# Kernel tuning notes

Hardware: AMD Instinct MI355X
Metric: run time of the kernel (lower is better)

Reference implementation:

```python
import jax, jax.numpy as jnp
import numpy as np

EPS_BN = 1e-5
EPS_COS = 1e-8

N, F_IN, HID, OUT, S, NNZ = 50000, 1024, 256, 280, 5000, 800000


def setup_inputs() -> dict:
    key = jax.random.key(0)
    ks = jax.random.split(key, 20)
    inp = {}
    inp["x"] = jax.random.normal(ks[0], (N, F_IN), jnp.float32)
    inp["y"] = jax.random.normal(ks[1], (S, OUT), jnp.float32)
    inp["adj_rows"] = jax.random.randint(ks[2], (NNZ,), 0, N, jnp.int32)
    inp["adj_cols"] = jax.random.randint(ks[3], (NNZ,), 0, N, jnp.int32)
    inp["adj_vals"] = jax.random.uniform(ks[4], (NNZ,), jnp.float32)
    inp["agg_rows"] = jax.random.randint(ks[5], (N,), 0, S, jnp.int32)
    inp["agg_vals"] = jax.random.uniform(ks[6], (N,), jnp.float32)
    inp["perm"] = jax.random.permutation(ks[7], N).astype(jnp.int32)
    # parameters (kaiming-ish scale)
    def lin(k, fi, fo):
        k1, k2 = jax.random.split(k)
        w = jax.random.normal(k1, (fi, fo), jnp.float32) / np.sqrt(fi)
        b = jax.random.normal(k2, (fo,), jnp.float32) * 0.01
        return w, b
    inp["mlp_W"], inp["mlp_b"] = lin(ks[8], F_IN, HID)
    inp["bn_gamma"] = jnp.ones((HID,), jnp.float32)
    inp["bn_beta"] = jnp.zeros((HID,), jnp.float32)
    inp["hg_W1"], inp["hg_b1"] = lin(ks[9], HID, HID)
    inp["hg_W2"], inp["hg_b2"] = lin(ks[10], HID, HID)
    inp["hg_prelu"] = jnp.float32(0.25)
    inp["pred_W"], inp["pred_b"] = lin(ks[11], HID, OUT)
    inp["dgi_W"], inp["dgi_b"] = lin(ks[12], HID, OUT)
    inp["dgi_prelu"] = jnp.float32(0.25)
    return inp


def _spmm(rows, cols, vals, M, n_out):
    # sparse(H) @ M : gather source rows, scale by edge value, scatter-add to dest
    return jax.ops.segment_sum(vals[:, None] * M[cols], rows, num_segments=n_out)


def _prelu(t, a):
    return jnp.where(t >= 0, t, a * t)


def _leaky(t, s):
    return jnp.where(t >= 0, t, s * t)


def reference(x, y, adj_rows, adj_cols, adj_vals, agg_rows, agg_vals, perm,
              mlp_W, mlp_b, bn_gamma, bn_beta, hg_W1, hg_b1, hg_W2, hg_b2,
              hg_prelu, pred_W, pred_b, dgi_W, dgi_b, dgi_prelu):
    n = x.shape[0]
    s = y.shape[0]
    # mlp: Linear -> LeakyReLU(0.1) -> BatchNorm1d (batch stats, training mode)
    h0 = _leaky(x @ mlp_W + mlp_b, 0.1)
    mu = jnp.mean(h0, axis=0)
    var = jnp.mean((h0 - mu) ** 2, axis=0)  # biased, as torch BN training
    h0 = bn_gamma * (h0 - mu) * jax.lax.rsqrt(var + EPS_BN) + bn_beta
    # HGNN, num_layers=2 (dropout = identity in eval)
    t = _spmm(adj_rows, adj_cols, adj_vals, h0 @ hg_W1 + hg_b1, n)
    t = _prelu(t, hg_prelu)
    t = _spmm(adj_rows, adj_cols, adj_vals, t @ hg_W2 + hg_b2, n)
    h = _leaky(t, 0.01)
    x_prime = _leaky(h @ pred_W + pred_b, 0.01)
    # Xenium: loss = MSE(agg_mtx @ x_prime, y); agg_mtx has one nnz per cell
    agg = jax.ops.segment_sum(agg_vals[:, None] * x_prime, agg_rows, num_segments=s)
    loss = jnp.mean((agg - y) ** 2)
    # DGI (1-layer HGNN with PReLU)
    h1 = _prelu(_spmm(adj_rows, adj_cols, adj_vals, h0 @ dgi_W + dgi_b, n), dgi_prelu)
    c = jnp.mean(h1, axis=0)  # (OUT,)
    h2 = _prelu(_spmm(adj_rows, adj_cols, adj_vals, h0[perm] @ dgi_W + dgi_b, n), dgi_prelu)
    c_norm = jnp.linalg.norm(c)
    def cos(hm):
        return (hm @ c) / jnp.maximum(jnp.linalg.norm(hm, axis=1) * c_norm, EPS_COS)
    loss = loss + jnp.mean(1.0 - cos(h1)) + jnp.mean(jnp.maximum(cos(h2), 0.0))
    return (loss, x_prime)
```

## Files before the change

### kernel.cpp

```cpp
#include <hip/hip_runtime.h>
#include <hip/hip_bf16.h>

#define DEVI __device__ __forceinline__

typedef __attribute__((ext_vector_type(8))) short short8;
typedef __attribute__((ext_vector_type(4))) float float4v;

DEVI float bf2f(__hip_bfloat16 v) { return __bfloat162float(v); }
DEVI float ldbs(const ushort* p, size_t i) { return bf2f(((const __hip_bfloat16*)p)[i]); }
DEVI ushort f2bs(float v) {
    __hip_bfloat16 h = __float2bfloat16(v);
    return *(ushort*)&h;
}
DEVI float bfs2f(short s) {
    ushort u = (ushort)s;
    return bf2f(*(__hip_bfloat16*)&u);
}

DEVI float ldin(const void* p, size_t i, int isf32) {
    return isf32 ? ((const float*)p)[i] : bf2f(((const __hip_bfloat16*)p)[i]);
}
DEVI void stio(void* p, size_t i, float v, int isf32) {
    if (isf32) ((float*)p)[i] = v;
    else ((ushort*)p)[i] = f2bs(v);
}

template <int ACT>
DEVI float act_fn(float v, float alpha) {
    if (ACT == 1) return v >= 0.f ? v : 0.1f * v;
    if (ACT == 2) return v >= 0.f ? v : 0.01f * v;
    if (ACT == 3) return v >= 0.f ? v : alpha * v;
    return v;
}

DEVI float waveRed(float v) {
#pragma unroll
    for (int o = 32; o > 0; o >>= 1) v += __shfl_down(v, o);
    return v;
}

DEVI float blockRed(float v) {
    __shared__ float sm[16];
    int lane = threadIdx.x & 63, w = threadIdx.x >> 6;
    v = waveRed(v);
    if (lane == 0) sm[w] = v;
    __syncthreads();
    if (w == 0) {
        int nw = (blockDim.x + 63) >> 6;
        v = (lane < nw) ? sm[lane] : 0.f;
        v = waveRed(v);
    }
    return v;
}

__global__ void probe_k(const void* __restrict__ x, int* __restrict__ flag) {
    __shared__ int sfails;
    int t = threadIdx.x;
    if (t == 0) sfails = 0;
    __syncthreads();
    const __hip_bfloat16* xb = (const __hip_bfloat16*)x;
    int my = 0;
    for (int i = t; i < 4096; i += 256) {
        float v = bf2f(xb[i]);
        float a = fabsf(v);
        if (!(a <= 64.f) || (v != 0.f && a < 1e-6f)) my++;
    }
    atomicAdd(&sfails, my);
    __syncthreads();
    if (t == 0) flag[0] = (sfails > 409) ? 1 : 0;
}

struct Cvt5 {
    const void* src[5];
    ushort* dst[5];
    int K[5];
    int N[5];
};
__global__ void cvt_all_k(Cvt5 d, const int* __restrict__ flagp) {
    int f32 = flagp[0];
    int seg = blockIdx.y;
    int idx = blockIdx.x * blockDim.x + threadIdx.x;
    int K = d.K[seg], Nc = d.N[seg];
    int total = K * Nc;
    if (idx < total) {
        int k = idx / Nc, n = idx % Nc;
        d.dst[seg][(size_t)n * K + k] = f2bs(ldin(d.src[seg], idx, f32));
    }
}

#define TP 40
template <int AMODE, int ACT, int OMODE>
__global__ __launch_bounds__(256) void mgemm_k(
    const void* __restrict__ A, const ushort* __restrict__ Bt,
    const void* __restrict__ bias, void* __restrict__ outp, ushort* __restrict__ outp2,
    const int* __restrict__ flagp, int M, int K, int Nc) {
    __shared__ short As[128 * TP];
    __shared__ short Bs[128 * TP];
    const int f32 = flagp[0];
    const int tid = threadIdx.x;
    const int lane = tid & 63;
    const int l15 = lane & 15;
    const int quad = lane >> 4;
    const int wid = tid >> 6;
    const int mW = (wid >> 1) * 64;
    const int nW = (wid & 1) * 64;
    const int mBase = blockIdx.x * 128;
    const int nBase = blockIdx.y * 128;

    float4v acc[4][4];
#pragma unroll
    for (int i = 0; i < 4; i++)
#pragma unroll
        for (int j = 0; j < 4; j++) acc[i][j] = (float4v){0.f, 0.f, 0.f, 0.f};

    for (int k0 = 0; k0 < K; k0 += 32) {
#pragma unroll
        for (int i = 0; i < 2; i++) {
            int chunk = i * 256 + tid;
            int row = chunk >> 2;
            int c = chunk & 3;
            short8 va = {0, 0, 0, 0, 0, 0, 0, 0};
            int gr = mBase + row;
            if (gr < M) {
                size_t ge = (size_t)gr * K + k0 + c * 8;
                if (AMODE == 1 || !f32) {
                    va = *(const short8*)((const ushort*)A + ge);
                } else {
                    const float* af = (const float*)A + ge;
#pragma unroll
                    for (int j = 0; j < 8; j++) va[j] = (short)f2bs(af[j]);
                }
            }
            *(short8*)&As[row * TP + c * 8] = va;

            short8 vb = {0, 0, 0, 0, 0, 0, 0, 0};
            int gn = nBase + row;
            if (gn < Nc) vb = *(const short8*)(Bt + (size_t)gn * K + k0 + c * 8);
            *(short8*)&Bs[row * TP + c * 8] = vb;
        }
        __syncthreads();

        short8 af[4], bf[4];
#pragma unroll
        for (int i = 0; i < 4; i++)
            af[i] = *(const short8*)&As[(mW + i * 16 + l15) * TP + quad * 8];
#pragma unroll
        for (int j = 0; j < 4; j++)
            bf[j] = *(const short8*)&Bs[(nW + j * 16 + l15) * TP + quad * 8];
#pragma unroll
        for (int i = 0; i < 4; i++)
#pragma unroll
            for (int j = 0; j < 4; j++)
                acc[i][j] =
                    __builtin_amdgcn_mfma_f32_16x16x32_bf16(af[i], bf[j], acc[i][j], 0, 0, 0);
        __syncthreads();
    }

#pragma unroll
    for (int i = 0; i < 4; i++) {
#pragma unroll
        for (int j = 0; j < 4; j++) {
            int gcn = nBase + nW + j * 16 + l15;
            if (gcn >= Nc) continue;
            float bv = ldin(bias, gcn, f32);
#pragma unroll
            for (int r = 0; r < 4; r++) {
                int grm = mBase + mW + i * 16 + quad * 4 + r;
                if (grm >= M) continue;
                float v = act_fn<ACT>(acc[i][j][r] + bv, 0.f);
                size_t oi = (size_t)grm * Nc + gcn;
                if (OMODE == 1) {
                    stio(outp, 1 + oi, v, f32);
                    outp2[oi] = f2bs(v);
                } else {
                    ((ushort*)outp)[oi] = f2bs(v);
                }
            }
        }
    }
}

__global__ void count_k(const int* __restrict__ rows, int* __restrict__ counts, int nnz) {
    int i = blockIdx.x * blockDim.x + threadIdx.x;
    if (i < nnz) atomicAdd(&counts[rows[i]], 1);
}

__global__ __launch_bounds__(1024) void scan_local_k(const int* __restrict__ counts,
                                                     int* __restrict__ offs,
                                                     int* __restrict__ bsums, int n) {
    __shared__ int sm[1024];
    int t = threadIdx.x;
    int g = blockIdx.x * 1024 + t;
    int v = (g < n) ? counts[g] : 0;
    sm[t] = v;
    __syncthreads();
    for (int d = 1; d < 1024; d <<= 1) {
        int add = (t >= d) ? sm[t - d] : 0;
        __syncthreads();
        sm[t] += add;
        __syncthreads();
    }
    if (g < n) offs[g] = sm[t] - v;
    if (t == 1023) bsums[blockIdx.x] = sm[t];
}

__global__ void scan_bsums_k(int* bsums, int nb) {
    if (threadIdx.x == 0 && blockIdx.x == 0) {
        int acc = 0;
        for (int i = 0; i < nb; i++) {
            int v = bsums[i];
            bsums[i] = acc;
            acc += v;
        }
    }
}

__global__ void scan_add_k(int* __restrict__ offs, const int* __restrict__ bsums, int n, int nnz) {
    int g = blockIdx.x * blockDim.x + threadIdx.x;
    if (g < n) offs[g] += bsums[g >> 10];
    if (g == 0) offs[n] = nnz;
}

__global__ void fill_k(const int* __restrict__ rows, const int* __restrict__ cols,
                       const void* __restrict__ vals, const int* __restrict__ perm,
                       const int* __restrict__ offs, int* __restrict__ cursor,
                       int* __restrict__ cols_s, int* __restrict__ colsp_s,
                       float* __restrict__ vals_s, const int* __restrict__ flagp, int nnz) {
    int e = blockIdx.x * blockDim.x + threadIdx.x;
    if (e < nnz) {
        int r = rows[e];
        int pos = offs[r] + atomicAdd(&cursor[r], 1);
        int c = cols[e];
        cols_s[pos] = c;
        colsp_s[pos] = perm[c];
        vals_s[pos] = ldin(vals, e, flagp[0]);
    }
}

__global__ void fill_s_k(const int* __restrict__ rows, const void* __restrict__ vals,
                         const int* __restrict__ offs, int* __restrict__ cursor,
                         int* __restrict__ idx_s, float* __restrict__ val_s,
                         const int* __restrict__ flagp, int n) {
    int e = blockIdx.x * blockDim.x + threadIdx.x;
    if (e < n) {
        int r = rows[e];
        int pos = offs[r] + atomicAdd(&cursor[r], 1);
        idx_s[pos] = e;
        val_s[pos] = ldin(vals, e, flagp[0]);
    }
}

template <int ACT, bool DUAL>
__global__ __launch_bounds__(256) void spmmv_k(
    const int* __restrict__ offs, const int* __restrict__ cols_s,
    const int* __restrict__ colsp_s, const float* __restrict__ vals_s,
    const void* __restrict__ alpha_p, const int* __restrict__ flagp,
    const ushort* __restrict__ Min, ushort* __restrict__ out1, ushort* __restrict__ out2,
    int Nrow, int F) {
    int row = blockIdx.x * 4 + (threadIdx.x >> 6);
    if (row >= Nrow) return;
    int lane = threadIdx.x & 63;
    int half = lane >> 5, l5 = lane & 31;
    int FC = F >> 3;
    bool has1 = (l5 + 32) < FC;
    float alpha = (ACT == 3) ? ldin(alpha_p, 0, flagp[0]) : 0.f;
    int s = offs[row], e = offs[row + 1];
    float a0[8] = {}, a1[8] = {}, b0[8] = {}, b1[8] = {};
#pragma unroll 2
    for (int i = s + half; i < e; i += 2) {
        float v = vals_s[i];
        int c = cols_s[i];
        const ushort* src = Min + (size_t)c * F;
        short8 h = *(const short8*)(src + l5 * 8);
#pragma unroll
        for (int j = 0; j < 8; j++) a0[j] += v * bfs2f(h[j]);
        if (has1) {
            short8 h2 = *(const short8*)(src + (l5 + 32) * 8);
#pragma unroll
            for (int j = 0; j < 8; j++) a1[j] += v * bfs2f(h2[j]);
        }
        if (DUAL) {
            int cp = colsp_s[i];
            const ushort* srcp = Min + (size_t)cp * F;
            short8 g = *(const short8*)(srcp + l5 * 8);
#pragma unroll
            for (int j = 0; j < 8; j++) b0[j] += v * bfs2f(g[j]);
            if (has1) {
                short8 g2 = *(const short8*)(srcp + (l5 + 32) * 8);
#pragma unroll
                for (int j = 0; j < 8; j++) b1[j] += v * bfs2f(g2[j]);
            }
        }
    }
#pragma unroll
    for (int j = 0; j < 8; j++) {
        a0[j] += __shfl_xor(a0[j], 32);
        if (has1) a1[j] += __shfl_xor(a1[j], 32);
        if (DUAL) {
            b0[j] += __shfl_xor(b0[j], 32);
            if (has1) b1[j] += __shfl_xor(b1[j], 32);
        }
    }
    if (half == 0) {
        short8 o;
        size_t base = (size_t)row * F;
#pragma unroll
        for (int j = 0; j < 8; j++) o[j] = (short)f2bs(act_fn<ACT>(a0[j], alpha));
        *(short8*)(out1 + base + l5 * 8) = o;
        if (has1) {
#pragma unroll
            for (int j = 0; j < 8; j++) o[j] = (short)f2bs(act_fn<ACT>(a1[j], alpha));
            *(short8*)(out1 + base + (l5 + 32) * 8) = o;
        }
        if (DUAL) {
#pragma unroll
            for (int j = 0; j < 8; j++) o[j] = (short)f2bs(act_fn<ACT>(b0[j], alpha));
            *(short8*)(out2 + base + l5 * 8) = o;
            if (has1) {
#pragma unroll
                for (int j = 0; j < 8; j++) o[j] = (short)f2bs(act_fn<ACT>(b1[j], alpha));
                *(short8*)(out2 + base + (l5 + 32) * 8) = o;
            }
        }
    }
}

__global__ __launch_bounds__(256) void aggmse_k(
    const int* __restrict__ soffs, const int* __restrict__ sidx, const float* __restrict__ sval,
    const ushort* __restrict__ xp, const void* __restrict__ y, const int* __restrict__ flagp,
    float* __restrict__ lacc, int S, int F) {
    int srow = blockIdx.x * 4 + (threadIdx.x >> 6);
    int lane = threadIdx.x & 63;
    int half = lane >> 5, l5 = lane & 31;
    int FC = F >> 3;
    bool has1 = (l5 + 32) < FC;
    float a0[8] = {}, a1[8] = {};
    if (srow < S) {
        int s = soffs[srow], e = soffs[srow + 1];
        for (int i = s + half; i < e; i += 2) {
            float v = sval[i];
            int n = sidx[i];
            const ushort* src = xp + (size_t)n * F;
            short8 h = *(const short8*)(src + l5 * 8);
#pragma unroll
            for (int j = 0; j < 8; j++) a0[j] += v * bfs2f(h[j]);
            if (has1) {
                short8 h2 = *(const short8*)(src + (l5 + 32) * 8);
#pragma unroll
                for (int j = 0; j < 8; j++) a1[j] += v * bfs2f(h2[j]);
            }
        }
    }
#pragma unroll
    for (int j = 0; j < 8; j++) {
        a0[j] += __shfl_xor(a0[j], 32);
        if (has1) a1[j] += __shfl_xor(a1[j], 32);
    }
    float ss = 0.f;
    if (srow < S && half == 0) {
        int f32 = flagp[0];
        size_t base = (size_t)srow * F;
#pragma unroll
        for (int j = 0; j < 8; j++) {
            float d = a0[j] - ldin(y, base + l5 * 8 + j, f32);
            ss += d * d;
        }
        if (has1) {
#pragma unroll
            for (int j = 0; j < 8; j++) {
                float d = a1[j] - ldin(y, base + (l5 + 32) * 8 + j, f32);
                ss += d * d;
            }
        }
    }
    ss = blockRed(ss);
    if (threadIdx.x == 0) atomicAdd(&lacc[0], ss);
}

__global__ __launch_bounds__(256) void bn_stats_k(const ushort* __restrict__ h,
                                                  float* __restrict__ sum,
                                                  float* __restrict__ sumsq, int nrows, int rpb) {
    int c = threadIdx.x;
    int rs = blockIdx.x * rpb;
    int re = min(rs + rpb, nrows);
    float s = 0.f, s2 = 0.f;
    int H = blockDim.x;
    for (int r = rs; r < re; r++) {
        float v = ldbs(h, (size_t)r * H + c);
        s += v;
        s2 += v * v;
    }
    atomicAdd(&sum[c], s);
    atomicAdd(&sumsq[c], s2);
}

__global__ void bn_final_k(const float* __restrict__ sum, const float* __restrict__ sumsq,
                           const void* __restrict__ gamma, const void* __restrict__ beta,
                           float* __restrict__ scale, float* __restrict__ shift,
                           const int* __restrict__ flagp, int nrows) {
    int c = threadIdx.x;
    int f32 = flagp[0];
    float mu = sum[c] / nrows;
    float var = sumsq[c] / nrows - mu * mu;
    float sc = ldin(gamma, c, f32) * rsqrtf(var + 1e-5f);
    scale[c] = sc;
    shift[c] = ldin(beta, c, f32) - mu * sc;
}

__global__ void bn_apply_k(ushort* __restrict__ h, const float* __restrict__ scale,
                           const float* __restrict__ shift) {
    int c = threadIdx.x;
    int H = blockDim.x;
    size_t i = (size_t)blockIdx.x * H + c;
    h[i] = f2bs(ldbs(h, i) * scale[c] + shift[c]);
}

__global__ __launch_bounds__(320) void colsum_k(const ushort* __restrict__ h,
                                                float* __restrict__ accum, int nrows, int F,
                                                int rpb) {
    int f = threadIdx.x;
    if (f >= F) return;
    int rs = blockIdx.x * rpb;
    int re = min(rs + rpb, nrows);
    float s = 0.f;
    for (int r = rs; r < re; r++) s += ldbs(h, (size_t)r * F + f);
    atomicAdd(&accum[f], s);
}

__global__ __launch_bounds__(320) void cfinal_k(const float* __restrict__ accum,
                                                float* __restrict__ c, float* __restrict__ cnorm,
                                                int N, int F) {
    int f = threadIdx.x;
    float v = 0.f;
    if (f < F) {
        v = accum[f] / N;
        c[f] = v;
    }
    float s2 = blockRed(v * v);
    if (threadIdx.x == 0) cnorm[0] = sqrtf(s2);
}

template <int MODE>
__global__ __launch_bounds__(256) void cos_k(const ushort* __restrict__ h,
                                             const float* __restrict__ c,
                                             const float* __restrict__ cnorm,
                                             float* __restrict__ acc, int N, int F) {
    int gw = (blockIdx.x * blockDim.x + threadIdx.x) >> 6;
    int lane = threadIdx.x & 63;
    int nw = (gridDim.x * blockDim.x) >> 6;
    float cn = cnorm[0];
    float s = 0.f;
    for (int row = gw; row < N; row += nw) {
        float dot = 0.f, nsq = 0.f;
        for (int f = lane; f < F; f += 64) {
            float v = ldbs(h, (size_t)row * F + f);
            dot += v * c[f];
            nsq += v * v;
        }
#pragma unroll
        for (int o = 32; o > 0; o >>= 1) {
            dot += __shfl_down(dot, o);
            nsq += __shfl_down(nsq, o);
        }
        if (lane == 0) {
            float cosv = dot / fmaxf(sqrtf(nsq) * cn, 1e-8f);
            s += (MODE == 1) ? fmaxf(cosv, 0.f) : cosv;
        }
    }
    s = blockRed(s);
    if (threadIdx.x == 0) atomicAdd(acc, s);
}

__global__ void final_k(const float* __restrict__ lacc, void* __restrict__ dout,
                        const int* __restrict__ flagp, int SOUT, int N) {
    if (threadIdx.x == 0 && blockIdx.x == 0) {
        float loss = lacc[0] / SOUT + (1.f - lacc[1] / N) + lacc[2] / N;
        stio(dout, 0, loss, flagp[0]);
    }
}

extern "C" void kernel_launch(void* const* d_in, const int* in_sizes, int n_in,
                              void* d_out, int out_size, void* d_ws, size_t ws_size,
                              hipStream_t stream) {
    const void* x = d_in[0];
    const void* y = d_in[1];
    const int* adj_rows = (const int*)d_in[2];
    const int* adj_cols = (const int*)d_in[3];
    const void* adj_vals = d_in[4];
    const int* agg_rows = (const int*)d_in[5];
    const void* agg_vals = d_in[6];
    const int* perm = (const int*)d_in[7];
    const void* mlp_W = d_in[8];
    const void* mlp_b = d_in[9];
    const void* bn_gamma = d_in[10];
    const void* bn_beta = d_in[11];
    const void* hg_W1 = d_in[12];
    const void* hg_b1 = d_in[13];
    const void* hg_W2 = d_in[14];
    const void* hg_b2 = d_in[15];
    const void* hg_prelu = d_in[16];
    const void* pred_W = d_in[17];
    const void* pred_b = d_in[18];
    const void* dgi_W = d_in[19];
    const void* dgi_b = d_in[20];
    const void* dgi_prelu = d_in[21];

    const int N = in_sizes[5];
    const int NNZ = in_sizes[2];
    const int F_IN = in_sizes[0] / N;
    const int HID = in_sizes[9];
    const int OUT = in_sizes[18];
    const int S = in_sizes[1] / OUT;

    char* w = (char*)d_ws;
    size_t off = 0;
    auto alloc = [&](size_t b) -> char* {
        char* p = w + off;
        off += (b + 255) & ~(size_t)255;
        return p;
    };
    ushort* h0_bf = (ushort*)alloc((size_t)N * HID * 2);
    ushort* zA_bf = (ushort*)alloc((size_t)N * OUT * 2);
    ushort* zB_bf = (ushort*)alloc((size_t)N * OUT * 2);
    ushort* h2_bf = (ushort*)alloc((size_t)N * OUT * 2);
    ushort* xp_ws = (ushort*)alloc((size_t)N * OUT * 2);
    ushort* mlpWt = (ushort*)alloc((size_t)HID * F_IN * 2);
    ushort* hgW1t = (ushort*)alloc((size_t)HID * HID * 2);
    ushort* hgW2t = (ushort*)alloc((size_t)HID * HID * 2);
    ushort* predWt = (ushort*)alloc((size_t)OUT * HID * 2);
    ushort* dgiWt = (ushort*)alloc((size_t)OUT * HID * 2);
    int* offs = (int*)alloc((size_t)(N + 1) * 4);
    int nbscan = (N + 1023) / 1024;
    int* bsums = (int*)alloc((size_t)nbscan * 4);
    int* cols_s = (int*)alloc((size_t)NNZ * 4);
    int* colsp_s = (int*)alloc((size_t)NNZ * 4);
    float* vals_s = (float*)alloc((size_t)NNZ * 4);
    int* soffs = (int*)alloc((size_t)(S + 1) * 4);
    int nbscan_s = (S + 1023) / 1024;
    int* sbsums = (int*)alloc((size_t)nbscan_s * 4);
    int* sidx = (int*)alloc((size_t)N * 4);
    float* sval = (float*)alloc((size_t)N * 4);
    float* bn_scale = (float*)alloc((size_t)HID * 4);
    float* bn_shift = (float*)alloc((size_t)HID * 4);
    float* c_vec = (float*)alloc((size_t)OUT * 4);
    float* cnorm = (float*)alloc(4);
    int* dflag = (int*)alloc(16);
    char* zero_base = w + off;
    int* counts = (int*)alloc((size_t)N * 4);
    int* cursor = (int*)alloc((size_t)N * 4);
    int* scnt = (int*)alloc((size_t)S * 4);
    int* scursor = (int*)alloc((size_t)S * 4);
    float* bn_sum = (float*)alloc((size_t)HID * 4);
    float* bn_sumsq = (float*)alloc((size_t)HID * 4);
    float* c_acc = (float*)alloc((size_t)OUT * 4);
    float* lacc = (float*)alloc(16);
    size_t zero_bytes = (w + off) - zero_base;
    hipMemsetAsync(zero_base, 0, zero_bytes, stream);

    probe_k<<<1, 256, 0, stream>>>(x, dflag);

    Cvt5 cv;
    cv.src[0] = mlp_W;  cv.dst[0] = mlpWt;  cv.K[0] = F_IN; cv.N[0] = HID;
    cv.src[1] = hg_W1;  cv.dst[1] = hgW1t;  cv.K[1] = HID;  cv.N[1] = HID;
    cv.src[2] = hg_W2;  cv.dst[2] = hgW2t;  cv.K[2] = HID;  cv.N[2] = HID;
    cv.src[3] = pred_W; cv.dst[3] = predWt; cv.K[3] = HID;  cv.N[3] = OUT;
    cv.src[4] = dgi_W;  cv.dst[4] = dgiWt;  cv.K[4] = HID;  cv.N[4] = OUT;
    cvt_all_k<<<dim3((F_IN * HID + 255) / 256, 5), 256, 0, stream>>>(cv, dflag);

    count_k<<<(NNZ + 255) / 256, 256, 0, stream>>>(adj_rows, counts, NNZ);
    scan_local_k<<<nbscan, 1024, 0, stream>>>(counts, offs, bsums, N);
    scan_bsums_k<<<1, 64, 0, stream>>>(bsums, nbscan);
    scan_add_k<<<(N + 255) / 256, 256, 0, stream>>>(offs, bsums, N, NNZ);
    fill_k<<<(NNZ + 255) / 256, 256, 0, stream>>>(adj_rows, adj_cols, adj_vals, perm, offs,
                                                  cursor, cols_s, colsp_s, vals_s, dflag, NNZ);
    count_k<<<(N + 255) / 256, 256, 0, stream>>>(agg_rows, scnt, N);
    scan_local_k<<<nbscan_s, 1024, 0, stream>>>(scnt, soffs, sbsums, S);
    scan_bsums_k<<<1, 64, 0, stream>>>(sbsums, nbscan_s);
    scan_add_k<<<(S + 255) / 256, 256, 0, stream>>>(soffs, sbsums, S, N);
    fill_s_k<<<(N + 255) / 256, 256, 0, stream>>>(agg_rows, agg_vals, soffs, scursor, sidx, sval,
                                                  dflag, N);

    const int MT = (N + 127) / 128;
    const int SPB = (N + 3) / 4;
    mgemm_k<0, 1, 0><<<dim3(MT, (HID + 127) / 128), 256, 0, stream>>>(x, mlpWt, mlp_b, h0_bf,
                                                                      nullptr, dflag, N, F_IN, HID);
    bn_stats_k<<<(N + 127) / 128, HID, 0, stream>>>(h0_bf, bn_sum, bn_sumsq, N, 128);
    bn_final_k<<<1, HID, 0, stream>>>(bn_sum, bn_sumsq, bn_gamma, bn_beta, bn_scale, bn_shift,
                                      dflag, N);
    bn_apply_k<<<N, HID, 0, stream>>>(h0_bf, bn_scale, bn_shift);

    mgemm_k<1, 0, 0><<<dim3(MT, (HID + 127) / 128), 256, 0, stream>>>(h0_bf, hgW1t, hg_b1, zA_bf,
                                                                      nullptr, dflag, N, HID, HID);
    spmmv_k<3, false><<<SPB, 256, 0, stream>>>(offs, cols_s, colsp_s, vals_s, hg_prelu, dflag,
                                               zA_bf, zB_bf, nullptr, N, HID);
    mgemm_k<1, 0, 0><<<dim3(MT, (HID + 127) / 128), 256, 0, stream>>>(zB_bf, hgW2t, hg_b2, zA_bf,
                                                                      nullptr, dflag, N, HID, HID);
    spmmv_k<2, false><<<SPB, 256, 0, stream>>>(offs, cols_s, colsp_s, vals_s, nullptr, dflag,
                                               zA_bf, zB_bf, nullptr, N, HID);

    mgemm_k<1, 2, 1><<<dim3(MT, (OUT + 127) / 128), 256, 0, stream>>>(zB_bf, predWt, pred_b, d_out,
                                                                      xp_ws, dflag, N, HID, OUT);
    aggmse_k<<<(S + 3) / 4, 256, 0, stream>>>(soffs, sidx, sval, xp_ws, y, dflag, lacc, S, OUT);

    mgemm_k<1, 0, 0><<<dim3(MT, (OUT + 127) / 128), 256, 0, stream>>>(h0_bf, dgiWt, dgi_b, zA_bf,
                                                                      nullptr, dflag, N, HID, OUT);
    spmmv_k<3, true><<<SPB, 256, 0, stream>>>(offs, cols_s, colsp_s, vals_s, dgi_prelu, dflag,
                                              zA_bf, zB_bf, h2_bf, N, OUT);
    colsum_k<<<(N + 127) / 128, 320, 0, stream>>>(zB_bf, c_acc, N, OUT, 128);
    cfinal_k<<<1, 320, 0, stream>>>(c_acc, c_vec, cnorm, N, OUT);
    cos_k<0><<<256, 256, 0, stream>>>(zB_bf, c_vec, cnorm, &lacc[1], N, OUT);
    cos_k<1><<<256, 256, 0, stream>>>(h2_bf, c_vec, cnorm, &lacc[2], N, OUT);

    final_k<<<1, 64, 0, stream>>>(lacc, d_out, dflag, S * OUT, N);
}
```

Measured before the change: 1.362 ms.

## Batch SpMM gathers, vectorize BN apply and fp32 loads, pad OUT stride

The SpMM inner loop now issues several independent row gathers before accumulating, to hide gather latency. BN apply is vectorized to 8 bf16 elements per thread, replacing the one-block-per-row launch. The fp32 A-tile load uses float4 reads, and the GEMM grid swaps axes so N-tiles of the same M rows run adjacently. The intermediate buffer with OUT columns gets a 64-aligned row stride, and xp_ws now shares that buffer, which saves memory but depends on stage ordering to stay correct.

Measured after the change: 1.357 ms. About the same (-0.4%).

```diff
diff --git a/kernel.cpp b/kernel.cpp
--- a/kernel.cpp
+++ b/kernel.cpp
@@ -93,7 +93,7 @@
 __global__ __launch_bounds__(256) void mgemm_k(
     const void* __restrict__ A, const ushort* __restrict__ Bt,
     const void* __restrict__ bias, void* __restrict__ outp, ushort* __restrict__ outp2,
-    const int* __restrict__ flagp, int M, int K, int Nc) {
+    const int* __restrict__ flagp, int M, int K, int Nc, int LDo) {
     __shared__ short As[128 * TP];
     __shared__ short Bs[128 * TP];
     const int f32 = flagp[0];
@@ -104,8 +104,8 @@
     const int wid = tid >> 6;
     const int mW = (wid >> 1) * 64;
     const int nW = (wid & 1) * 64;
-    const int mBase = blockIdx.x * 128;
-    const int nBase = blockIdx.y * 128;
+    const int mBase = blockIdx.y * 128;
+    const int nBase = blockIdx.x * 128;
 
     float4v acc[4][4];
 #pragma unroll
@@ -127,8 +127,12 @@
                     va = *(const short8*)((const ushort*)A + ge);
                 } else {
                     const float* af = (const float*)A + ge;
-#pragma unroll
-                    for (int j = 0; j < 8; j++) va[j] = (short)f2bs(af[j]);
+                    float4v f0 = *(const float4v*)af;
+                    float4v f1 = *(const float4v*)(af + 4);
+#pragma unroll
+                    for (int j = 0; j < 4; j++) va[j] = (short)f2bs(f0[j]);
+#pragma unroll
+                    for (int j = 0; j < 4; j++) va[4 + j] = (short)f2bs(f1[j]);
                 }
             }
             *(short8*)&As[row * TP + c * 8] = va;
@@ -168,12 +172,11 @@
                 int grm = mBase + mW + i * 16 + quad * 4 + r;
                 if (grm >= M) continue;
                 float v = act_fn<ACT>(acc[i][j][r] + bv, 0.f);
-                size_t oi = (size_t)grm * Nc + gcn;
                 if (OMODE == 1) {
-                    stio(outp, 1 + oi, v, f32);
-                    outp2[oi] = f2bs(v);
+                    stio(outp, 1 + (size_t)grm * Nc + gcn, v, f32);
+                    outp2[(size_t)grm * LDo + gcn] = f2bs(v);
                 } else {
-                    ((ushort*)outp)[oi] = f2bs(v);
+                    ((ushort*)outp)[(size_t)grm * LDo + gcn] = f2bs(v);
                 }
             }
         }
@@ -256,7 +259,7 @@
     const int* __restrict__ colsp_s, const float* __restrict__ vals_s,
     const void* __restrict__ alpha_p, const int* __restrict__ flagp,
     const ushort* __restrict__ Min, ushort* __restrict__ out1, ushort* __restrict__ out2,
-    int Nrow, int F) {
+    int Nrow, int F, int LDin) {
     int row = blockIdx.x * 4 + (threadIdx.x >> 6);
     if (row >= Nrow) return;
     int lane = threadIdx.x & 63;
@@ -266,11 +269,56 @@
     float alpha = (ACT == 3) ? ldin(alpha_p, 0, flagp[0]) : 0.f;
     int s = offs[row], e = offs[row + 1];
     float a0[8] = {}, a1[8] = {}, b0[8] = {}, b1[8] = {};
-#pragma unroll 2
-    for (int i = s + half; i < e; i += 2) {
+
+    constexpr int DEPTH = DUAL ? 2 : 4;
+    int i = s + half;
+    for (; i + 2 * (DEPTH - 1) < e; i += 2 * DEPTH) {
+        int c[DEPTH];
+        float v[DEPTH];
+        int cp[DEPTH];
+#pragma unroll
+        for (int u = 0; u < DEPTH; u++) {
+            c[u] = cols_s[i + 2 * u];
+            v[u] = vals_s[i + 2 * u];
+        }
+        if (DUAL) {
+#pragma unroll
+            for (int u = 0; u < DEPTH; u++) cp[u] = colsp_s[i + 2 * u];
+        }
+        short8 h0v[DEPTH], h1v[DEPTH], g0v[DEPTH], g1v[DEPTH];
+#pragma unroll
+        for (int u = 0; u < DEPTH; u++) {
+            const ushort* src = Min + (size_t)c[u] * LDin;
+            h0v[u] = *(const short8*)(src + l5 * 8);
+            if (has1) h1v[u] = *(const short8*)(src + (l5 + 32) * 8);
+            if (DUAL) {
+                const ushort* srcp = Min + (size_t)cp[u] * LDin;
+                g0v[u] = *(const short8*)(srcp + l5 * 8);
+                if (has1) g1v[u] = *(const short8*)(srcp + (l5 + 32) * 8);
+            }
+        }
+#pragma unroll
+        for (int u = 0; u < DEPTH; u++) {
+#pragma unroll
+            for (int j = 0; j < 8; j++) a0[j] += v[u] * bfs2f(h0v[u][j]);
+            if (has1) {
+#pragma unroll
+                for (int j = 0; j < 8; j++) a1[j] += v[u] * bfs2f(h1v[u][j]);
+            }
+            if (DUAL) {
+#pragma unroll
+                for (int j = 0; j < 8; j++) b0[j] += v[u] * bfs2f(g0v[u][j]);
+                if (has1) {
+#pragma unroll
+                    for (int j = 0; j < 8; j++) b1[j] += v[u] * bfs2f(g1v[u][j]);
+                }
+            }
+        }
+    }
+    for (; i < e; i += 2) {
         float v = vals_s[i];
         int c = cols_s[i];
-        const ushort* src = Min + (size_t)c * F;
+        const ushort* src = Min + (size_t)c * LDin;
         short8 h = *(const short8*)(src + l5 * 8);
 #pragma unroll
         for (int j = 0; j < 8; j++) a0[j] += v * bfs2f(h[j]);
@@ -281,7 +329,7 @@
         }
         if (DUAL) {
             int cp = colsp_s[i];
-            const ushort* srcp = Min + (size_t)cp * F;
+            const ushort* srcp = Min + (size_t)cp * LDin;
             short8 g = *(const short8*)(srcp + l5 * 8);
 #pragma unroll
             for (int j = 0; j < 8; j++) b0[j] += v * bfs2f(g[j]);
@@ -328,7 +376,7 @@
 __global__ __launch_bounds__(256) void aggmse_k(
     const int* __restrict__ soffs, const int* __restrict__ sidx, const float* __restrict__ sval,
     const ushort* __restrict__ xp, const void* __restrict__ y, const int* __restrict__ flagp,
-    float* __restrict__ lacc, int S, int F) {
+    float* __restrict__ lacc, int S, int F, int LDxp) {
     int srow = blockIdx.x * 4 + (threadIdx.x >> 6);
     int lane = threadIdx.x & 63;
     int half = lane >> 5, l5 = lane & 31;
@@ -340,7 +388,7 @@
         for (int i = s + half; i < e; i += 2) {
             float v = sval[i];
             int n = sidx[i];
-            const ushort* src = xp + (size_t)n * F;
+            const ushort* src = xp + (size_t)n * LDxp;
             short8 h = *(const short8*)(src + l5 * 8);
 #pragma unroll
             for (int j = 0; j < 8; j++) a0[j] += v * bfs2f(h[j]);
@@ -407,12 +455,19 @@
     shift[c] = ldin(beta, c, f32) - mu * sc;
 }
 
-__global__ void bn_apply_k(ushort* __restrict__ h, const float* __restrict__ scale,
-                           const float* __restrict__ shift) {
-    int c = threadIdx.x;
-    int H = blockDim.x;
-    size_t i = (size_t)blockIdx.x * H + c;
-    h[i] = f2bs(ldbs(h, i) * scale[c] + shift[c]);
+__global__ __launch_bounds__(256) void bn_apply_k(ushort* __restrict__ h,
+                                                  const float* __restrict__ scale,
+                                                  const float* __restrict__ shift, int total8,
+                                                  int H) {
+    int idx = blockIdx.x * 256 + threadIdx.x;
+    if (idx >= total8) return;
+    size_t base = (size_t)idx * 8;
+    int c = (int)(base % H);
+    short8 v = *(short8*)(h + base);
+    short8 o;
+#pragma unroll
+    for (int j = 0; j < 8; j++) o[j] = (short)f2bs(bfs2f(v[j]) * scale[c + j] + shift[c + j]);
+    *(short8*)(h + base) = o;
 }
 
 __global__ __launch_bounds__(320) void colsum_k(const ushort* __restrict__ h,
@@ -512,6 +567,8 @@
     const int OUT = in_sizes[18];
     const int S = in_sizes[1] / OUT;
 
+    const int LDP = (OUT + 63) & ~63;
+
     char* w = (char*)d_ws;
     size_t off = 0;
     auto alloc = [&](size_t b) -> char* {
@@ -520,10 +577,10 @@
         return p;
     };
     ushort* h0_bf = (ushort*)alloc((size_t)N * HID * 2);
-    ushort* zA_bf = (ushort*)alloc((size_t)N * OUT * 2);
+    ushort* zA_bf = (ushort*)alloc((size_t)N * LDP * 2);
     ushort* zB_bf = (ushort*)alloc((size_t)N * OUT * 2);
     ushort* h2_bf = (ushort*)alloc((size_t)N * OUT * 2);
-    ushort* xp_ws = (ushort*)alloc((size_t)N * OUT * 2);
+    ushort* xp_ws = zA_bf;
     ushort* mlpWt = (ushort*)alloc((size_t)HID * F_IN * 2);
     ushort* hgW1t = (ushort*)alloc((size_t)HID * HID * 2);
     ushort* hgW2t = (ushort*)alloc((size_t)HID * HID * 2);
@@ -582,30 +639,35 @@
 
     const int MT = (N + 127) / 128;
     const int SPB = (N + 3) / 4;
-    mgemm_k<0, 1, 0><<<dim3(MT, (HID + 127) / 128), 256, 0, stream>>>(x, mlpWt, mlp_b, h0_bf,
-                                                                      nullptr, dflag, N, F_IN, HID);
+    mgemm_k<0, 1, 0><<<dim3((HID + 127) / 128, MT), 256, 0, stream>>>(
+        x, mlpWt, mlp_b, h0_bf, nullptr, dflag, N, F_IN, HID, HID);
     bn_stats_k<<<(N + 127) / 128, HID, 0, stream>>>(h0_bf, bn_sum, bn_sumsq, N, 128);
     bn_final_k<<<1, HID, 0, stream>>>(bn_sum, bn_sumsq, bn_gamma, bn_beta, bn_scale, bn_shift,
                                       dflag, N);
-    bn_apply_k<<<N, HID, 0, stream>>>(h0_bf, bn_scale, bn_shift);
-
-    mgemm_k<1, 0, 0><<<dim3(MT, (HID + 127) / 128), 256, 0, stream>>>(h0_bf, hgW1t, hg_b1, zA_bf,
-                                                                      nullptr, dflag, N, HID, HID);
+    {
+        int total8 = (N * HID) / 8;
+        bn_apply_k<<<(total8 + 255) / 256, 256, 0, stream>>>(h0_bf, bn_scale, bn_shift, total8,
+                                                             HID);
+    }
+
+    mgemm_k<1, 0, 0><<<dim3((HID + 127) / 128, MT), 256, 0, stream>>>(
+        h0_bf, hgW1t, hg_b1, zA_bf, nullptr, dflag, N, HID, HID, HID);
     spmmv_k<3, false><<<SPB, 256, 0, stream>>>(offs, cols_s, colsp_s, vals_s, hg_prelu, dflag,
-                                               zA_bf, zB_bf, nullptr, N, HID);
-    mgemm_k<1, 0, 0><<<dim3(MT, (HID + 127) / 128), 256, 0, stream>>>(zB_bf, hgW2t, hg_b2, zA_bf,
-                                                                      nullptr, dflag, N, HID, HID);
+                                               zA_bf, zB_bf, nullptr, N, HID, HID);
+    mgemm_k<1, 0, 0><<<dim3((HID + 127) / 128, MT), 256, 0, stream>>>(
+        zB_bf, hgW2t, hg_b2, zA_bf, nullptr, dflag, N, HID, HID, HID);
     spmmv_k<2, false><<<SPB, 256, 0, stream>>>(offs, cols_s, colsp_s, vals_s, nullptr, dflag,
-                                               zA_bf, zB_bf, nullptr, N, HID);
-
-    mgemm_k<1, 2, 1><<<dim3(MT, (OUT + 127) / 128), 256, 0, stream>>>(zB_bf, predWt, pred_b, d_out,
-                                                                      xp_ws, dflag, N, HID, OUT);
-    aggmse_k<<<(S + 3) / 4, 256, 0, stream>>>(soffs, sidx, sval, xp_ws, y, dflag, lacc, S, OUT);
-
-    mgemm_k<1, 0, 0><<<dim3(MT, (OUT + 127) / 128), 256, 0, stream>>>(h0_bf, dgiWt, dgi_b, zA_bf,
-                                                                      nullptr, dflag, N, HID, OUT);
+                                               zA_bf, zB_bf, nullptr, N, HID, HID);
+
+    mgemm_k<1, 2, 1><<<dim3((OUT + 127) / 128, MT), 256, 0, stream>>>(
+        zB_bf, predWt, pred_b, d_out, xp_ws, dflag, N, HID, OUT, LDP);
+    aggmse_k<<<(S + 3) / 4, 256, 0, stream>>>(soffs, sidx, sval, xp_ws, y, dflag, lacc, S, OUT,
+                                              LDP);
+
+    mgemm_k<1, 0, 0><<<dim3((OUT + 127) / 128, MT), 256, 0, stream>>>(
+        h0_bf, dgiWt, dgi_b, zA_bf, nullptr, dflag, N, HID, OUT, LDP);
     spmmv_k<3, true><<<SPB, 256, 0, stream>>>(offs, cols_s, colsp_s, vals_s, dgi_prelu, dflag,
-                                              zA_bf, zB_bf, h2_bf, N, OUT);
+                                              zA_bf, zB_bf, h2_bf, N, OUT, LDP);
     colsum_k<<<(N + 127) / 128, 320, 0, stream>>>(zB_bf, c_acc, N, OUT, 128);
     cfinal_k<<<1, 320, 0, stream>>>(c_acc, c_vec, cnorm, N, OUT);
     cos_k<0><<<256, 256, 0, stream>>>(zB_bf, c_vec, cnorm, &lacc[1], N, OUT);
```
